# Performance work log

Measured on AMD Instinct MI355X. Metric: run time of the kernel, lower is better.

## Reference

```python
import jax, jax.numpy as jnp
import numpy as np
from jax import lax

B, S, D, E, K, MULT = 4, 2048, 1024, 1536, 4, 4
LN_EPS = 1e-5

def log_g(x):
    return jnp.where(x >= 0, jnp.log(jax.nn.relu(x) + 0.5), -jax.nn.softplus(-x))

def layer_norm(x, g, b):
    mu = jnp.mean(x, axis=-1, keepdims=True)
    var = jnp.mean((x - mu) ** 2, axis=-1, keepdims=True)
    return (x - mu) * lax.rsqrt(var + LN_EPS) * g + b

def setup_inputs() -> dict:
    key = jax.random.key(0)
    ks = jax.random.split(key, 16)
    s = lambda fan: 1.0 / np.sqrt(fan)
    inp = {
        'x': jax.random.normal(ks[0], (B, S, D), dtype=jnp.float32),
        'conv_dw_w': jax.random.uniform(ks[1], (D, 1, K), jnp.float32, -s(K), s(K)),
        'conv_dw_b': jax.random.uniform(ks[2], (D,), jnp.float32, -s(K), s(K)),
        'conv_pw_w': jax.random.uniform(ks[3], (D, D), jnp.float32, -s(D), s(D)),
        'conv_pw_b': jax.random.uniform(ks[4], (D,), jnp.float32, -s(D), s(D)),
        'ln1_g': jnp.ones((D,), jnp.float32),
        'ln1_b': jnp.zeros((D,), jnp.float32),
        'w_f': jax.random.uniform(ks[5], (E, D), jnp.float32, -s(D), s(D)),
        'w_i': jax.random.uniform(ks[6], (E, D), jnp.float32, -s(D), s(D)),
        'w_h': jax.random.uniform(ks[7], (E, D), jnp.float32, -s(D), s(D)),
        'w_down': jax.random.uniform(ks[8], (D, E), jnp.float32, -s(E), s(E)),
        'ln2_g': jnp.ones((D,), jnp.float32),
        'ln2_b': jnp.zeros((D,), jnp.float32),
        'mlp_w1': jax.random.uniform(ks[9], (MULT * D, D), jnp.float32, -s(D), s(D)),
        'mlp_b1': jax.random.uniform(ks[10], (MULT * D,), jnp.float32, -s(D), s(D)),
        'mlp_w2': jax.random.uniform(ks[11], (D, MULT * D), jnp.float32, -s(MULT * D), s(MULT * D)),
        'mlp_b2': jax.random.uniform(ks[12], (D,), jnp.float32, -s(MULT * D), s(MULT * D)),
    }
    return inp

def _forward(x, conv_dw_w, conv_dw_b, conv_pw_w, conv_pw_b, ln1_g, ln1_b,
             w_f, w_i, w_h, w_down, ln2_g, ln2_b, mlp_w1, mlp_b1, mlp_w2, mlp_b2):
    residual = x
    # causal depthwise conv + pointwise conv (channels-first over time)
    xc = jnp.transpose(x, (0, 2, 1))                       # (B, D, S)
    xc = jnp.pad(xc, ((0, 0), (0, 0), (K - 1, 0)))         # left causal pad
    dw = lax.conv_general_dilated(xc, conv_dw_w, (1,), 'VALID',
                                  feature_group_count=D,
                                  dimension_numbers=('NCH', 'OIH', 'NCH'))
    dw = dw + conv_dw_b[None, :, None]
    pw = jnp.einsum('bds,ed->bes', dw, conv_pw_w) + conv_pw_b[None, :, None]
    x = jnp.transpose(pw, (0, 2, 1)) + residual
    x = layer_norm(x, ln1_g, ln1_b)
    # minLSTM log-space parallel scan
    log_f = -jax.nn.softplus(-(x @ w_f.T))                 # (B, S, E)
    log_i = -jax.nn.softplus(-(x @ w_i.T))
    log_th = log_g(x @ w_h.T)
    log_h0 = jnp.full((B, 1, E), jnp.log(jnp.float32(0.5)), dtype=x.dtype)
    log_values = jnp.concatenate([log_h0, log_i + log_th], axis=1)   # (B, S+1, E)
    a_star = jnp.pad(jnp.cumsum(log_f, axis=1), ((0, 0), (1, 0), (0, 0)))
    log_h = a_star + lax.cumlogsumexp(log_values - a_star, axis=1)
    h = jnp.exp(log_h)[:, 1:]                              # (B, S, E)
    x = h @ w_down.T + residual
    x = layer_norm(x, ln2_g, ln2_b)
    # MLP (exact GELU like torch default); dropout with p=0 is identity
    hmid = jax.nn.gelu(x @ mlp_w1.T + mlp_b1, approximate=False)
    return hmid @ mlp_w2.T + mlp_b2

def reference(x, conv_dw_w, conv_dw_b, conv_pw_w, conv_pw_b, ln1_g, ln1_b,
              w_f, w_i, w_h, w_down, ln2_g, ln2_b, mlp_w1, mlp_b1, mlp_w2, mlp_b2):
    return _forward(x, conv_dw_w, conv_dw_b, conv_pw_w, conv_pw_b, ln1_g, ln1_b,
                    w_f, w_i, w_h, w_down, ln2_g, ln2_b, mlp_w1, mlp_b1, mlp_w2, mlp_b2)
```

## Files before the change

kernel.cpp:

```cpp
#include <hip/hip_runtime.h>
#include <hip/hip_bf16.h>
#include <math.h>

using bf16 = __hip_bfloat16;
typedef __attribute__((ext_vector_type(8))) short s8v;
typedef __attribute__((ext_vector_type(4))) float f32x4;

#define B_  4
#define S_  2048
#define D_  1024
#define E_  1536
#define M_  (B_*S_)
#define BE_ (B_*E_)
#define NCH 16
#define CHS (S_/NCH)

__device__ __forceinline__ float b2f(bf16 h) { return __bfloat162float(h); }
__device__ __forceinline__ bf16  f2b(float f) { return __float2bfloat16(f); }

struct __align__(8)  bh4 { bf16 h[4]; };

__device__ __forceinline__ void gld16(const void* g, void* l) {
  __builtin_amdgcn_global_load_lds((const __attribute__((address_space(1))) void*)g,
                                   (__attribute__((address_space(3))) void*)l, 16, 0, 0);
}

__global__ __launch_bounds__(256) void cvt_k(const float* __restrict__ s,
                                             bf16* __restrict__ d, int n)
{
  int i = (blockIdx.x * 256 + threadIdx.x) * 4;
  if (i < n) {
    float4 v = *(const float4*)(s + i);
    bh4 o;
    o.h[0] = f2b(v.x); o.h[1] = f2b(v.y); o.h[2] = f2b(v.z); o.h[3] = f2b(v.w);
    *(bh4*)(d + i) = o;
  }
}

__global__ __launch_bounds__(256) void dwconv_k(const float* __restrict__ x,
                                                const float* __restrict__ w,
                                                const float* __restrict__ bias,
                                                bf16* __restrict__ out)
{
  int m = blockIdx.x;
  int s = m & (S_ - 1);
  int d = threadIdx.x * 4;
  float wf[4][4];
#pragma unroll
  for (int i = 0; i < 4; ++i) {
    float4 wr = *(const float4*)(w + (d + i) * 4);
    wf[i][0] = wr.x; wf[i][1] = wr.y; wf[i][2] = wr.z; wf[i][3] = wr.w;
  }
  float4 bb = *(const float4*)(bias + d);
  float acc[4] = {bb.x, bb.y, bb.z, bb.w};
#pragma unroll
  for (int k = 0; k < 4; ++k) {
    if (s - 3 + k >= 0) {
      float4 xv = *(const float4*)(x + (size_t)(m - 3 + k) * D_ + d);
      acc[0] += xv.x * wf[0][k];
      acc[1] += xv.y * wf[1][k];
      acc[2] += xv.z * wf[2][k];
      acc[3] += xv.w * wf[3][k];
    }
  }
  bh4 ov;
#pragma unroll
  for (int i = 0; i < 4; ++i) ov.h[i] = f2b(acc[i]);
  *(bh4*)(out + (size_t)m * D_ + d) = ov;
}

template<int EPI>
__global__ __launch_bounds__(256) void gemm_ab(const bf16* __restrict__ A, int lda,
                                               const bf16* __restrict__ Bb, int ldb,
                                               const float* __restrict__ bias,
                                               const float* __restrict__ resid,
                                               bf16* outH, bf16* outH2, float* outF,
                                               int M, int N, int K)
{
  __shared__ __align__(16) bf16 lsA[128 * 64];
  __shared__ __align__(16) bf16 lsB[128 * 64];
  const int tid  = threadIdx.x;
  const int lane = tid & 63;
  const int wave = tid >> 6;
  const int m0 = blockIdx.y * 128, n0 = blockIdx.x * 128;
  const int wm = (wave >> 1) * 64, wn = (wave & 1) * 64;
  const int r = lane & 15, q = lane >> 4;
  const int sw = r & 7;
  f32x4 acc[4][4] = {};

  for (int k0 = 0; k0 < K; k0 += 64) {
#pragma unroll
    for (int i = 0; i < 4; ++i) {
      int c = i * 256 + tid;
      int row = c >> 3, cc = (c & 7) ^ (row & 7);
      gld16(A  + (size_t)(m0 + row) * lda + k0 + cc * 8, (char*)lsA + c * 16);
      gld16(Bb + (size_t)(n0 + row) * ldb + k0 + cc * 8, (char*)lsB + c * 16);
    }
    __syncthreads();
#pragma unroll
    for (int kk = 0; kk < 64; kk += 32) {
      const int j = (kk >> 3) + q;
      s8v af[4], bfr[4];
#pragma unroll
      for (int t = 0; t < 4; ++t) {
        af[t]  = *(const s8v*)((char*)lsA + (((wm + t * 16 + r) << 3) + (j ^ sw)) * 16);
        bfr[t] = *(const s8v*)((char*)lsB + (((wn + t * 16 + r) << 3) + (j ^ sw)) * 16);
      }
#pragma unroll
      for (int mi = 0; mi < 4; ++mi)
#pragma unroll
        for (int ni = 0; ni < 4; ++ni)
          acc[mi][ni] = __builtin_amdgcn_mfma_f32_16x16x32_bf16(af[mi], bfr[ni], acc[mi][ni], 0, 0, 0);
    }
    __syncthreads();
  }

#pragma unroll
  for (int mi = 0; mi < 4; ++mi) {
#pragma unroll
    for (int j = 0; j < 4; ++j) {
      int row = m0 + wm + mi * 16 + q * 4 + j;
#pragma unroll
      for (int ni = 0; ni < 4; ++ni) {
        int col = n0 + wn + ni * 16 + r;
        size_t idx = (size_t)row * N + col;
        float v = acc[mi][ni][j];
        if constexpr (EPI == 0) {
          outH[idx] = f2b(v + bias[col] + resid[idx]);
        } else if constexpr (EPI == 1) {
          if (col < 1536) outH [(size_t)row * 1536 + col]        = f2b(v);
          else            outH2[(size_t)row * 1536 + col - 1536] = f2b(v);
        } else if constexpr (EPI == 2) {
          float gh = (v >= 0.f) ? (v + 0.5f) : (1.f / (1.f + expf(-v)));
          float iv = 1.f / (1.f + expf(-b2f(outH[idx])));
          outH[idx] = f2b(gh * iv);
        } else if constexpr (EPI == 3) {
          outH[idx] = f2b(v + resid[idx]);
        } else if constexpr (EPI == 4) {
          float u = v + bias[col];
          outH[idx] = f2b(0.5f * u * (1.f + erff(u * 0.70710678118f)));
        } else {
          outF[idx] = v + bias[col];
        }
      }
    }
  }
}

__global__ __launch_bounds__(256) void ln_k(const bf16* __restrict__ y,
                                            const float* __restrict__ g,
                                            const float* __restrict__ b,
                                            bf16* __restrict__ out)
{
  __shared__ float sm[8];
  int row = blockIdx.x;
  bh4 v4 = ((const bh4*)(y + (size_t)row * D_))[threadIdx.x];
  float v0 = b2f(v4.h[0]), v1 = b2f(v4.h[1]), v2 = b2f(v4.h[2]), v3 = b2f(v4.h[3]);
  float s = v0 + v1 + v2 + v3;
#pragma unroll
  for (int o = 32; o; o >>= 1) s += __shfl_down(s, o);
  int lane = threadIdx.x & 63, w = threadIdx.x >> 6;
  if (lane == 0) sm[w] = s;
  __syncthreads();
  float mu = (sm[0] + sm[1] + sm[2] + sm[3]) * (1.f / D_);
  float d0 = v0 - mu, d1 = v1 - mu, d2 = v2 - mu, d3 = v3 - mu;
  float qq = d0 * d0 + d1 * d1 + d2 * d2 + d3 * d3;
#pragma unroll
  for (int o = 32; o; o >>= 1) qq += __shfl_down(qq, o);
  if (lane == 0) sm[4 + w] = qq;
  __syncthreads();
  float var = (sm[4] + sm[5] + sm[6] + sm[7]) * (1.f / D_);
  float inv = rsqrtf(var + 1e-5f);
  int c = threadIdx.x * 4;
  float4 gv = *(const float4*)(g + c);
  float4 bv = *(const float4*)(b + c);
  bh4 ov;
  ov.h[0] = f2b(d0 * inv * gv.x + bv.x);
  ov.h[1] = f2b(d1 * inv * gv.y + bv.y);
  ov.h[2] = f2b(d2 * inv * gv.z + bv.z);
  ov.h[3] = f2b(d3 * inv * gv.w + bv.w);
  *(bh4*)(out + (size_t)row * D_ + c) = ov;
}

__global__ __launch_bounds__(256) void scanA2_k(const bf16* __restrict__ fpre,
                                                const bf16* __restrict__ g,
                                                float* __restrict__ Fc, float* __restrict__ Gc)
{
  int gth = blockIdx.x * 256 + threadIdx.x;
  int c = gth / BE_, be = gth % BE_;
  int b = be / E_,  e = be % E_;
  size_t idx = (size_t)b * S_ * E_ + (size_t)c * CHS * E_ + e;
  float F = 1.f, G = 0.f;
  for (int sl = 0; sl < CHS; ++sl, idx += E_) {
    float fv = 1.f / (1.f + expf(-b2f(fpre[idx])));
    F *= fv;
    G = fv * G + b2f(g[idx]);
  }
  Fc[gth] = F; Gc[gth] = G;
}

__global__ __launch_bounds__(256) void scanB_k(const float* __restrict__ Fc,
                                               const float* __restrict__ Gc,
                                               float* __restrict__ hst)
{
  int be = blockIdx.x * 256 + threadIdx.x;
  float h = 0.5f;
#pragma unroll
  for (int c = 0; c < NCH; ++c) {
    hst[c * BE_ + be] = h;
    h = Fc[c * BE_ + be] * h + Gc[c * BE_ + be];
  }
}

__global__ __launch_bounds__(256) void scanC2_k(const bf16* __restrict__ fpre,
                                                bf16* g,
                                                const float* __restrict__ hst)
{
  int gth = blockIdx.x * 256 + threadIdx.x;
  int c = gth / BE_, be = gth % BE_;
  int b = be / E_,  e = be % E_;
  size_t idx = (size_t)b * S_ * E_ + (size_t)c * CHS * E_ + e;
  float h = hst[gth];
  for (int sl = 0; sl < CHS; ++sl, idx += E_) {
    float fv = 1.f / (1.f + expf(-b2f(fpre[idx])));
    h = fv * h + b2f(g[idx]);
    g[idx] = f2b(h);
  }
}

extern "C" void kernel_launch(void* const* d_in, const int* in_sizes, int n_in,
                              void* d_out, int out_size, void* d_ws, size_t ws_size,
                              hipStream_t stream)
{
  (void)in_sizes; (void)n_in; (void)out_size; (void)ws_size;
  const float* x      = (const float*)d_in[0];
  const float* cdw_w  = (const float*)d_in[1];
  const float* cdw_b  = (const float*)d_in[2];
  const float* cpw_w  = (const float*)d_in[3];
  const float* cpw_b  = (const float*)d_in[4];
  const float* ln1_g  = (const float*)d_in[5];
  const float* ln1_b  = (const float*)d_in[6];
  const float* w_f    = (const float*)d_in[7];
  const float* w_i    = (const float*)d_in[8];
  const float* w_h    = (const float*)d_in[9];
  const float* w_down = (const float*)d_in[10];
  const float* ln2_g  = (const float*)d_in[11];
  const float* ln2_b  = (const float*)d_in[12];
  const float* mlp_w1 = (const float*)d_in[13];
  const float* mlp_b1 = (const float*)d_in[14];
  const float* mlp_w2 = (const float*)d_in[15];
  const float* mlp_b2 = (const float*)d_in[16];
  char* ws = (char*)d_ws;
  float* outF = (float*)d_out;

  bf16* dw_buf = (bf16*)(ws + 0);
  bf16* xln    = (bf16*)(ws + 0);
  float* Fc    = (float*)(ws + 0);
  float* Gc    = (float*)(ws + 393216);
  float* hst   = (float*)(ws + 786432);
  bf16* yb     = (bf16*)(ws + 16777216);
  bf16* hmid   = (bf16*)(ws + 16777216);
  bf16* fpre   = (bf16*)(ws + 33554432);
  bf16* gvals  = (bf16*)(ws + 58720256);
  bf16* pwb    = (bf16*)(ws + 83886080);
  bf16* wfib   = (bf16*)(ws + 85983232);
  bf16* whb    = (bf16*)(ws + 92274688);
  bf16* wdb    = (bf16*)(ws + 95420416);
  bf16* w1b    = (bf16*)(ws + 98566144);
  bf16* w2b    = (bf16*)(ws + 106954752);

  cvt_k<<<(D_*D_)/1024,   256, 0, stream>>>(cpw_w,  pwb, D_*D_);
  cvt_k<<<(E_*D_)/1024,   256, 0, stream>>>(w_f,    wfib, E_*D_);
  cvt_k<<<(E_*D_)/1024,   256, 0, stream>>>(w_i,    wfib + E_*D_, E_*D_);
  cvt_k<<<(E_*D_)/1024,   256, 0, stream>>>(w_h,    whb, E_*D_);
  cvt_k<<<(D_*E_)/1024,   256, 0, stream>>>(w_down, wdb, D_*E_);
  cvt_k<<<(4*D_*D_)/1024, 256, 0, stream>>>(mlp_w1, w1b, 4*D_*D_);
  cvt_k<<<(4*D_*D_)/1024, 256, 0, stream>>>(mlp_w2, w2b, 4*D_*D_);

  dwconv_k<<<M_, 256, 0, stream>>>(x, cdw_w, cdw_b, dw_buf);
  gemm_ab<0><<<dim3(8, 64), 256, 0, stream>>>(dw_buf, D_, pwb, D_, cpw_b, x, yb, nullptr, nullptr, M_, D_, D_);
  ln_k<<<M_, 256, 0, stream>>>(yb, ln1_g, ln1_b, xln);
  gemm_ab<1><<<dim3(24, 64), 256, 0, stream>>>(xln, D_, wfib, D_, nullptr, nullptr, fpre, gvals, nullptr, M_, 3072, D_);
  gemm_ab<2><<<dim3(12, 64), 256, 0, stream>>>(xln, D_, whb, D_, nullptr, nullptr, gvals, nullptr, nullptr, M_, E_, D_);
  scanA2_k<<<(BE_*NCH)/256, 256, 0, stream>>>(fpre, gvals, Fc, Gc);
  scanB_k<<<BE_/256, 256, 0, stream>>>(Fc, Gc, hst);
  scanC2_k<<<(BE_*NCH)/256, 256, 0, stream>>>(fpre, gvals, hst);
  gemm_ab<3><<<dim3(8, 64), 256, 0, stream>>>(gvals, E_, wdb, E_, nullptr, x, yb, nullptr, nullptr, M_, D_, E_);
  ln_k<<<M_, 256, 0, stream>>>(yb, ln2_g, ln2_b, xln);
  gemm_ab<4><<<dim3(32, 64), 256, 0, stream>>>(xln, D_, w1b, D_, mlp_b1, nullptr, hmid, nullptr, nullptr, M_, 4*D_, D_);
  gemm_ab<5><<<dim3(8, 64), 256, 0, stream>>>(hmid, 4*D_, w2b, 4*D_, mlp_b2, nullptr, nullptr, nullptr, outF, M_, D_, 4*D_);
}
```

Before: 658.1 us.

## Add 256x256-tile 8-wave phased GEMM for gate and MLP-up projections

Introduces a new bf16 MFMA GEMM kernel with 256x256 block tiles, 512 threads, double-buffered LDS via direct global-to-LDS loads, and a four-phase inner loop. That loop interleaves the next tile's loads with MFMA work under raised wave priority. It replaces the earlier GEMM for the f/i, h and MLP-up projections to raise arithmetic intensity and overlap memory with compute. The cost is 128KB of LDS per block, limiting occupancy to one block per CU. Grid sizes of 384 and 192 blocks may also leave CUs idle or create tail waves.

```diff
diff --git a/kernel.cpp b/kernel.cpp
--- a/kernel.cpp
+++ b/kernel.cpp
@@ -147,6 +147,169 @@
   }
 }
 
+__device__ __forceinline__ void mfma_ph(f32x4 (*ac)[4], const s8v af[2][2], const s8v bf[4][2]) {
+  __builtin_amdgcn_s_setprio(1);
+#pragma unroll
+  for (int kc = 0; kc < 2; ++kc)
+#pragma unroll
+    for (int mm = 0; mm < 2; ++mm)
+#pragma unroll
+      for (int n = 0; n < 4; ++n)
+        ac[mm][n] = __builtin_amdgcn_mfma_f32_16x16x32_bf16(af[mm][kc], bf[n][kc], ac[mm][n], 0, 0, 0);
+  __builtin_amdgcn_s_setprio(0);
+}
+
+template<int EPI>
+__global__ __launch_bounds__(512, 2) void gemm8p(const bf16* __restrict__ A, int lda,
+                                                 const bf16* __restrict__ Bb, int ldb,
+                                                 const float* __restrict__ bias,
+                                                 const float* __restrict__ resid,
+                                                 bf16* outH, bf16* outH2, float* outF,
+                                                 int M, int N, int K)
+{
+  __shared__ __align__(16) bf16 lsA[2][256 * 64];
+  __shared__ __align__(16) bf16 lsB[2][256 * 64];
+  const int tid  = threadIdx.x;
+  const int lane = tid & 63;
+  const int wave = tid >> 6;
+  const int q = lane >> 4, r = lane & 15;
+  const int wm = (wave >> 2) * 128;
+  const int wn = (wave & 3) * 64;
+  const int s0 = q ^ (r & 7);
+  const int s0b  = s0 << 4;
+  const int s0b4 = (s0 ^ 4) << 4;
+  const int m0 = blockIdx.y * 256, n0 = blockIdx.x * 256;
+  const int NT = K >> 6;
+
+  f32x4 acc[8][4] = {};
+  s8v af[2][2], bf4[4][2];
+
+  auto stB = [&](int h, int tn, int nb) {
+#pragma unroll
+    for (int i = 0; i < 2; ++i) {
+      int c  = (i << 9) + tid;
+      int rw = (h << 7) + (c >> 3);
+      int cc = (c & 7) ^ ((c >> 3) & 7);
+      gld16(Bb + (unsigned)((n0 + rw) * ldb + (tn << 6) + (cc << 3)),
+            (char*)lsB[nb] + (((h << 10) + c) << 4));
+    }
+  };
+  auto stA = [&](int h, int tn, int nb) {
+#pragma unroll
+    for (int i = 0; i < 2; ++i) {
+      int c   = (i << 9) + tid;
+      int sub = c >> 3;
+      int rw  = (sub & 63) + ((sub >> 6) << 7) + (h << 6);
+      int cc  = (c & 7) ^ (sub & 7);
+      gld16(A + (unsigned)((m0 + rw) * lda + (tn << 6) + (cc << 3)),
+            (char*)lsA[nb] + (((rw << 3) + (c & 7)) << 4));
+    }
+  };
+
+  stB(0, 0, 0); stB(1, 0, 0); stA(0, 0, 0); stA(1, 0, 0);
+
+  for (int t = 0; t < NT; ++t) {
+    const int cb = t & 1, nb = cb ^ 1;
+    const int tn = (t + 1 < NT) ? t + 1 : t;
+    const char* lsAc = (const char*)lsA[cb];
+    const char* lsBc = (const char*)lsB[cb];
+
+    asm volatile("s_waitcnt vmcnt(2)" ::: "memory");
+    __builtin_amdgcn_s_barrier();
+
+    {
+      const char* bb_ = lsBc + ((wn + r) << 7);
+#pragma unroll
+      for (int n = 0; n < 4; ++n) {
+        bf4[n][0] = *(const s8v*)(bb_ + n * 2048 + s0b);
+        bf4[n][1] = *(const s8v*)(bb_ + n * 2048 + s0b4);
+      }
+      const char* ab_ = lsAc + ((wm + r) << 7);
+      af[0][0] = *(const s8v*)(ab_ + s0b);
+      af[0][1] = *(const s8v*)(ab_ + s0b4);
+      af[1][0] = *(const s8v*)(ab_ + 2048 + s0b);
+      af[1][1] = *(const s8v*)(ab_ + 2048 + s0b4);
+    }
+    stB(0, tn, nb);
+    __builtin_amdgcn_s_barrier();
+    asm volatile("s_waitcnt lgkmcnt(0)" ::: "memory");
+    mfma_ph(&acc[0], af, bf4);
+    __builtin_amdgcn_s_barrier();
+
+    {
+      const char* ab_ = lsAc + ((wm + 32 + r) << 7);
+      af[0][0] = *(const s8v*)(ab_ + s0b);
+      af[0][1] = *(const s8v*)(ab_ + s0b4);
+      af[1][0] = *(const s8v*)(ab_ + 2048 + s0b);
+      af[1][1] = *(const s8v*)(ab_ + 2048 + s0b4);
+    }
+    stB(1, tn, nb);
+    __builtin_amdgcn_s_barrier();
+    asm volatile("s_waitcnt lgkmcnt(0)" ::: "memory");
+    mfma_ph(&acc[2], af, bf4);
+    asm volatile("s_waitcnt vmcnt(4)" ::: "memory");
+    __builtin_amdgcn_s_barrier();
+
+    {
+      const char* ab_ = lsAc + ((wm + 64 + r) << 7);
+      af[0][0] = *(const s8v*)(ab_ + s0b);
+      af[0][1] = *(const s8v*)(ab_ + s0b4);
+      af[1][0] = *(const s8v*)(ab_ + 2048 + s0b);
+      af[1][1] = *(const s8v*)(ab_ + 2048 + s0b4);
+    }
+    stA(0, tn, nb);
+    __builtin_amdgcn_s_barrier();
+    asm volatile("s_waitcnt lgkmcnt(0)" ::: "memory");
+    mfma_ph(&acc[4], af, bf4);
+    __builtin_amdgcn_s_barrier();
+
+    {
+      const char* ab_ = lsAc + ((wm + 96 + r) << 7);
+      af[0][0] = *(const s8v*)(ab_ + s0b);
+      af[0][1] = *(const s8v*)(ab_ + s0b4);
+      af[1][0] = *(const s8v*)(ab_ + 2048 + s0b);
+      af[1][1] = *(const s8v*)(ab_ + 2048 + s0b4);
+    }
+    stA(1, tn, nb);
+    __builtin_amdgcn_s_barrier();
+    asm volatile("s_waitcnt lgkmcnt(0)" ::: "memory");
+    mfma_ph(&acc[6], af, bf4);
+    __builtin_amdgcn_s_barrier();
+  }
+  asm volatile("s_waitcnt vmcnt(0)" ::: "memory");
+
+#pragma unroll
+  for (int mi = 0; mi < 8; ++mi) {
+#pragma unroll
+    for (int j = 0; j < 4; ++j) {
+      int row = m0 + wm + mi * 16 + q * 4 + j;
+#pragma unroll
+      for (int ni = 0; ni < 4; ++ni) {
+        int col = n0 + wn + ni * 16 + r;
+        size_t idx = (size_t)row * N + col;
+        float v = acc[mi][ni][j];
+        if constexpr (EPI == 0) {
+          outH[idx] = f2b(v + bias[col] + resid[idx]);
+        } else if constexpr (EPI == 1) {
+          if (col < 1536) outH [(size_t)row * 1536 + col]        = f2b(v);
+          else            outH2[(size_t)row * 1536 + col - 1536] = f2b(v);
+        } else if constexpr (EPI == 2) {
+          float gh = (v >= 0.f) ? (v + 0.5f) : (1.f / (1.f + expf(-v)));
+          float iv = 1.f / (1.f + expf(-b2f(outH[idx])));
+          outH[idx] = f2b(gh * iv);
+        } else if constexpr (EPI == 3) {
+          outH[idx] = f2b(v + resid[idx]);
+        } else if constexpr (EPI == 4) {
+          float u = v + bias[col];
+          outH[idx] = f2b(0.5f * u * (1.f + erff(u * 0.70710678118f)));
+        } else {
+          outF[idx] = v + bias[col];
+        }
+      }
+    }
+  }
+}
+
 __global__ __launch_bounds__(256) void ln_k(const bf16* __restrict__ y,
                                             const float* __restrict__ g,
                                             const float* __restrict__ b,
@@ -280,13 +443,13 @@
   dwconv_k<<<M_, 256, 0, stream>>>(x, cdw_w, cdw_b, dw_buf);
   gemm_ab<0><<<dim3(8, 64), 256, 0, stream>>>(dw_buf, D_, pwb, D_, cpw_b, x, yb, nullptr, nullptr, M_, D_, D_);
   ln_k<<<M_, 256, 0, stream>>>(yb, ln1_g, ln1_b, xln);
-  gemm_ab<1><<<dim3(24, 64), 256, 0, stream>>>(xln, D_, wfib, D_, nullptr, nullptr, fpre, gvals, nullptr, M_, 3072, D_);
-  gemm_ab<2><<<dim3(12, 64), 256, 0, stream>>>(xln, D_, whb, D_, nullptr, nullptr, gvals, nullptr, nullptr, M_, E_, D_);
+  gemm8p<1><<<dim3(12, 32), 512, 0, stream>>>(xln, D_, wfib, D_, nullptr, nullptr, fpre, gvals, nullptr, M_, 3072, D_);
+  gemm8p<2><<<dim3(6, 32),  512, 0, stream>>>(xln, D_, whb, D_, nullptr, nullptr, gvals, nullptr, nullptr, M_, E_, D_);
   scanA2_k<<<(BE_*NCH)/256, 256, 0, stream>>>(fpre, gvals, Fc, Gc);
   scanB_k<<<BE_/256, 256, 0, stream>>>(Fc, Gc, hst);
   scanC2_k<<<(BE_*NCH)/256, 256, 0, stream>>>(fpre, gvals, hst);
   gemm_ab<3><<<dim3(8, 64), 256, 0, stream>>>(gvals, E_, wdb, E_, nullptr, x, yb, nullptr, nullptr, M_, D_, E_);
   ln_k<<<M_, 256, 0, stream>>>(yb, ln2_g, ln2_b, xln);
-  gemm_ab<4><<<dim3(32, 64), 256, 0, stream>>>(xln, D_, w1b, D_, mlp_b1, nullptr, hmid, nullptr, nullptr, M_, 4*D_, D_);
+  gemm8p<4><<<dim3(16, 32), 512, 0, stream>>>(xln, D_, w1b, D_, mlp_b1, nullptr, hmid, nullptr, nullptr, M_, 4*D_, D_);
   gemm_ab<5><<<dim3(8, 64), 256, 0, stream>>>(hmid, 4*D_, w2b, 4*D_, mlp_b2, nullptr, nullptr, nullptr, outF, M_, D_, 4*D_);
 }
```

New measurement: 865.1 us. 1.31x slower.

## Double-buffer GEMM LDS loads with split A halves and merge weight converts

Applied to the files above, without the earlier changes.

The GEMM now double-buffers its LDS tiles. The next k-tile's B and A halves are issued through global_load_lds while MFMAs run on the current tile, and explicit vmcnt waits and barriers replace the two __syncthreads per iteration. The A tile load is split into two halves, interleaved with two MFMA phases under raised wave priority. The seven weight-conversion launches are merged into one kernel that dispatches on the flat index, which relies on the weight buffers being laid out contiguously in the workspace. Doubling LDS to 64KB per block and asking for 2 blocks per SM via launch bounds puts pressure on occupancy and registers.

```diff
diff --git a/kernel.cpp b/kernel.cpp
--- a/kernel.cpp
+++ b/kernel.cpp
@@ -25,16 +25,32 @@
                                    (__attribute__((address_space(3))) void*)l, 16, 0, 0);
 }
 
-__global__ __launch_bounds__(256) void cvt_k(const float* __restrict__ s,
-                                             bf16* __restrict__ d, int n)
-{
-  int i = (blockIdx.x * 256 + threadIdx.x) * 4;
-  if (i < n) {
-    float4 v = *(const float4*)(s + i);
-    bh4 o;
-    o.h[0] = f2b(v.x); o.h[1] = f2b(v.y); o.h[2] = f2b(v.z); o.h[3] = f2b(v.w);
-    *(bh4*)(d + i) = o;
-  }
+__global__ __launch_bounds__(256) void cvt7_k(const float* __restrict__ s0,
+                                              const float* __restrict__ s1,
+                                              const float* __restrict__ s2,
+                                              const float* __restrict__ s3,
+                                              const float* __restrict__ s4,
+                                              const float* __restrict__ s5,
+                                              const float* __restrict__ s6,
+                                              bf16* __restrict__ d)
+{
+  size_t i = ((size_t)blockIdx.x * 256 + threadIdx.x) * 4;
+  const float* s; size_t off;
+  if (i < 4194304) {
+    if (i < 1048576)      { s = s0; off = 0; }
+    else if (i < 2621440) { s = s1; off = 1048576; }
+    else                  { s = s2; off = 2621440; }
+  } else if (i < 7340032) {
+    if (i < 5767168)      { s = s3; off = 4194304; }
+    else                  { s = s4; off = 5767168; }
+  } else {
+    if (i < 11534336)     { s = s5; off = 7340032; }
+    else                  { s = s6; off = 11534336; }
+  }
+  float4 v = *(const float4*)(s + (i - off));
+  bh4 o;
+  o.h[0] = f2b(v.x); o.h[1] = f2b(v.y); o.h[2] = f2b(v.z); o.h[3] = f2b(v.w);
+  *(bh4*)(d + i) = o;
 }
 
 __global__ __launch_bounds__(256) void dwconv_k(const float* __restrict__ x,
@@ -70,15 +86,15 @@
 }
 
 template<int EPI>
-__global__ __launch_bounds__(256) void gemm_ab(const bf16* __restrict__ A, int lda,
-                                               const bf16* __restrict__ Bb, int ldb,
-                                               const float* __restrict__ bias,
-                                               const float* __restrict__ resid,
-                                               bf16* outH, bf16* outH2, float* outF,
-                                               int M, int N, int K)
-{
-  __shared__ __align__(16) bf16 lsA[128 * 64];
-  __shared__ __align__(16) bf16 lsB[128 * 64];
+__global__ __launch_bounds__(256, 2) void gemm_ab(const bf16* __restrict__ A, int lda,
+                                                  const bf16* __restrict__ Bb, int ldb,
+                                                  const float* __restrict__ bias,
+                                                  const float* __restrict__ resid,
+                                                  bf16* outH, bf16* outH2, float* outF,
+                                                  int M, int N, int K)
+{
+  __shared__ __align__(16) bf16 lsA[2][128 * 64];
+  __shared__ __align__(16) bf16 lsB[2][128 * 64];
   const int tid  = threadIdx.x;
   const int lane = tid & 63;
   const int wave = tid >> 6;
@@ -88,32 +104,79 @@
   const int sw = r & 7;
   f32x4 acc[4][4] = {};
 
-  for (int k0 = 0; k0 < K; k0 += 64) {
+  auto stB = [&](int tn, int nb) {
 #pragma unroll
     for (int i = 0; i < 4; ++i) {
       int c = i * 256 + tid;
       int row = c >> 3, cc = (c & 7) ^ (row & 7);
-      gld16(A  + (size_t)(m0 + row) * lda + k0 + cc * 8, (char*)lsA + c * 16);
-      gld16(Bb + (size_t)(n0 + row) * ldb + k0 + cc * 8, (char*)lsB + c * 16);
+      gld16(Bb + (size_t)(n0 + row) * ldb + tn * 64 + cc * 8, (char*)lsB[nb] + c * 16);
     }
-    __syncthreads();
-#pragma unroll
-    for (int kk = 0; kk < 64; kk += 32) {
-      const int j = (kk >> 3) + q;
-      s8v af[4], bfr[4];
-#pragma unroll
-      for (int t = 0; t < 4; ++t) {
-        af[t]  = *(const s8v*)((char*)lsA + (((wm + t * 16 + r) << 3) + (j ^ sw)) * 16);
-        bfr[t] = *(const s8v*)((char*)lsB + (((wn + t * 16 + r) << 3) + (j ^ sw)) * 16);
-      }
-#pragma unroll
-      for (int mi = 0; mi < 4; ++mi)
+  };
+  auto stA = [&](int h, int tn, int nb) {
+#pragma unroll
+    for (int i = 0; i < 2; ++i) {
+      int c = i * 256 + tid;
+      int sub = c >> 3;
+      int rw = (sub & 31) + ((sub >> 5) << 6) + h * 32;
+      int cc = (c & 7) ^ (sub & 7);
+      gld16(A + (size_t)(m0 + rw) * lda + tn * 64 + cc * 8,
+            (char*)lsA[nb] + (((rw << 3) + (c & 7)) << 4));
+    }
+  };
+
+  const int NT = K >> 6;
+  stB(0, 0); stA(0, 0, 0); stA(1, 0, 0);
+
+  for (int t = 0; t < NT; ++t) {
+    const int cb = t & 1, nb = cb ^ 1;
+    const int tn = (t + 1 < NT) ? (t + 1) : t;
+    const char* la = (const char*)lsA[cb];
+    const char* lb = (const char*)lsB[cb];
+
+    asm volatile("s_waitcnt vmcnt(2)" ::: "memory");
+    __builtin_amdgcn_s_barrier();
+    stB(tn, nb); stA(0, tn, nb);
+
+    s8v bfr[4][2], af[2][2];
+#pragma unroll
+    for (int ni = 0; ni < 4; ++ni)
+#pragma unroll
+      for (int kc = 0; kc < 2; ++kc)
+        bfr[ni][kc] = *(const s8v*)(lb + ((((wn + ni * 16 + r) << 3) + ((q + kc * 4) ^ sw)) << 4));
+#pragma unroll
+    for (int mi = 0; mi < 2; ++mi)
+#pragma unroll
+      for (int kc = 0; kc < 2; ++kc)
+        af[mi][kc] = *(const s8v*)(la + ((((wm + mi * 16 + r) << 3) + ((q + kc * 4) ^ sw)) << 4));
+    __builtin_amdgcn_s_setprio(1);
+#pragma unroll
+    for (int kc = 0; kc < 2; ++kc)
+#pragma unroll
+      for (int mi = 0; mi < 2; ++mi)
 #pragma unroll
         for (int ni = 0; ni < 4; ++ni)
-          acc[mi][ni] = __builtin_amdgcn_mfma_f32_16x16x32_bf16(af[mi], bfr[ni], acc[mi][ni], 0, 0, 0);
-    }
-    __syncthreads();
-  }
+          acc[mi][ni] = __builtin_amdgcn_mfma_f32_16x16x32_bf16(af[mi][kc], bfr[ni][kc], acc[mi][ni], 0, 0, 0);
+    __builtin_amdgcn_s_setprio(0);
+
+    asm volatile("s_waitcnt vmcnt(6)" ::: "memory");
+    __builtin_amdgcn_s_barrier();
+    stA(1, tn, nb);
+#pragma unroll
+    for (int mi = 0; mi < 2; ++mi)
+#pragma unroll
+      for (int kc = 0; kc < 2; ++kc)
+        af[mi][kc] = *(const s8v*)(la + ((((wm + (mi + 2) * 16 + r) << 3) + ((q + kc * 4) ^ sw)) << 4));
+    __builtin_amdgcn_s_setprio(1);
+#pragma unroll
+    for (int kc = 0; kc < 2; ++kc)
+#pragma unroll
+      for (int mi = 0; mi < 2; ++mi)
+#pragma unroll
+        for (int ni = 0; ni < 4; ++ni)
+          acc[mi + 2][ni] = __builtin_amdgcn_mfma_f32_16x16x32_bf16(af[mi][kc], bfr[ni][kc], acc[mi + 2][ni], 0, 0, 0);
+    __builtin_amdgcn_s_setprio(0);
+  }
+  asm volatile("s_waitcnt vmcnt(0)" ::: "memory");
 
 #pragma unroll
   for (int mi = 0; mi < 4; ++mi) {
@@ -269,13 +332,7 @@
   bf16* w1b    = (bf16*)(ws + 98566144);
   bf16* w2b    = (bf16*)(ws + 106954752);
 
-  cvt_k<<<(D_*D_)/1024,   256, 0, stream>>>(cpw_w,  pwb, D_*D_);
-  cvt_k<<<(E_*D_)/1024,   256, 0, stream>>>(w_f,    wfib, E_*D_);
-  cvt_k<<<(E_*D_)/1024,   256, 0, stream>>>(w_i,    wfib + E_*D_, E_*D_);
-  cvt_k<<<(E_*D_)/1024,   256, 0, stream>>>(w_h,    whb, E_*D_);
-  cvt_k<<<(D_*E_)/1024,   256, 0, stream>>>(w_down, wdb, D_*E_);
-  cvt_k<<<(4*D_*D_)/1024, 256, 0, stream>>>(mlp_w1, w1b, 4*D_*D_);
-  cvt_k<<<(4*D_*D_)/1024, 256, 0, stream>>>(mlp_w2, w2b, 4*D_*D_);
+  cvt7_k<<<15360, 256, 0, stream>>>(cpw_w, w_f, w_i, w_h, w_down, mlp_w1, mlp_w2, pwb);
 
   dwconv_k<<<M_, 256, 0, stream>>>(x, cdw_w, cdw_b, dw_buf);
   gemm_ab<0><<<dim3(8, 64), 256, 0, stream>>>(dw_buf, D_, pwb, D_, cpw_b, x, yb, nullptr, nullptr, M_, D_, D_);
```

Result: slower. 723.5 us (+9.9%).

## Add 128x256 wide GEMM tile for large-N GEMMs and fuse weight conversions

Applied to the files above, without the earlier changes.

Adds a 512-thread GEMM kernel with a 128x256 output tile, where 8 waves share one A tile, and uses it for the fused f/i projection, the h projection and the first MLP GEMM. The wider tile is meant to cut redundant A-tile global loads and raise MFMA work per barrier. It also merges the seven weight fp32-to-bf16 conversion launches into one kernel with range-based source selection, reducing launch overhead. The larger LDS footprint (48KB) and fewer blocks may reduce occupancy or leave the grid unevenly spread across CUs.

```diff
diff --git a/kernel.cpp b/kernel.cpp
--- a/kernel.cpp
+++ b/kernel.cpp
@@ -25,16 +25,32 @@
                                    (__attribute__((address_space(3))) void*)l, 16, 0, 0);
 }
 
-__global__ __launch_bounds__(256) void cvt_k(const float* __restrict__ s,
-                                             bf16* __restrict__ d, int n)
-{
-  int i = (blockIdx.x * 256 + threadIdx.x) * 4;
-  if (i < n) {
-    float4 v = *(const float4*)(s + i);
-    bh4 o;
-    o.h[0] = f2b(v.x); o.h[1] = f2b(v.y); o.h[2] = f2b(v.z); o.h[3] = f2b(v.w);
-    *(bh4*)(d + i) = o;
-  }
+__global__ __launch_bounds__(256) void cvt7_k(const float* __restrict__ s0,
+                                              const float* __restrict__ s1,
+                                              const float* __restrict__ s2,
+                                              const float* __restrict__ s3,
+                                              const float* __restrict__ s4,
+                                              const float* __restrict__ s5,
+                                              const float* __restrict__ s6,
+                                              bf16* __restrict__ d)
+{
+  size_t i = ((size_t)blockIdx.x * 256 + threadIdx.x) * 4;
+  const float* s; size_t off;
+  if (i < 4194304) {
+    if (i < 1048576)      { s = s0; off = 0; }
+    else if (i < 2621440) { s = s1; off = 1048576; }
+    else                  { s = s2; off = 2621440; }
+  } else if (i < 7340032) {
+    if (i < 5767168)      { s = s3; off = 4194304; }
+    else                  { s = s4; off = 5767168; }
+  } else {
+    if (i < 11534336)     { s = s5; off = 7340032; }
+    else                  { s = s6; off = 11534336; }
+  }
+  float4 v = *(const float4*)(s + (i - off));
+  bh4 o;
+  o.h[0] = f2b(v.x); o.h[1] = f2b(v.y); o.h[2] = f2b(v.z); o.h[3] = f2b(v.w);
+  *(bh4*)(d + i) = o;
 }
 
 __global__ __launch_bounds__(256) void dwconv_k(const float* __restrict__ x,
@@ -67,6 +83,32 @@
 #pragma unroll
   for (int i = 0; i < 4; ++i) ov.h[i] = f2b(acc[i]);
   *(bh4*)(out + (size_t)m * D_ + d) = ov;
+}
+
+template<int EPI>
+__device__ __forceinline__ void epi_store(float v, int row, int col, int N,
+                                          const float* __restrict__ bias,
+                                          const float* __restrict__ resid,
+                                          bf16* outH, bf16* outH2, float* outF)
+{
+  size_t idx = (size_t)row * N + col;
+  if constexpr (EPI == 0) {
+    outH[idx] = f2b(v + bias[col] + resid[idx]);
+  } else if constexpr (EPI == 1) {
+    if (col < 1536) outH [(size_t)row * 1536 + col]        = f2b(v);
+    else            outH2[(size_t)row * 1536 + col - 1536] = f2b(v);
+  } else if constexpr (EPI == 2) {
+    float gh = (v >= 0.f) ? (v + 0.5f) : (1.f / (1.f + expf(-v)));
+    float iv = 1.f / (1.f + expf(-b2f(outH[idx])));
+    outH[idx] = f2b(gh * iv);
+  } else if constexpr (EPI == 3) {
+    outH[idx] = f2b(v + resid[idx]);
+  } else if constexpr (EPI == 4) {
+    float u = v + bias[col];
+    outH[idx] = f2b(0.5f * u * (1.f + erff(u * 0.70710678118f)));
+  } else {
+    outF[idx] = v + bias[col];
+  }
 }
 
 template<int EPI>
@@ -116,35 +158,77 @@
   }
 
 #pragma unroll
-  for (int mi = 0; mi < 4; ++mi) {
+  for (int mi = 0; mi < 4; ++mi)
 #pragma unroll
     for (int j = 0; j < 4; ++j) {
       int row = m0 + wm + mi * 16 + q * 4 + j;
 #pragma unroll
-      for (int ni = 0; ni < 4; ++ni) {
-        int col = n0 + wn + ni * 16 + r;
-        size_t idx = (size_t)row * N + col;
-        float v = acc[mi][ni][j];
-        if constexpr (EPI == 0) {
-          outH[idx] = f2b(v + bias[col] + resid[idx]);
-        } else if constexpr (EPI == 1) {
-          if (col < 1536) outH [(size_t)row * 1536 + col]        = f2b(v);
-          else            outH2[(size_t)row * 1536 + col - 1536] = f2b(v);
-        } else if constexpr (EPI == 2) {
-          float gh = (v >= 0.f) ? (v + 0.5f) : (1.f / (1.f + expf(-v)));
-          float iv = 1.f / (1.f + expf(-b2f(outH[idx])));
-          outH[idx] = f2b(gh * iv);
-        } else if constexpr (EPI == 3) {
-          outH[idx] = f2b(v + resid[idx]);
-        } else if constexpr (EPI == 4) {
-          float u = v + bias[col];
-          outH[idx] = f2b(0.5f * u * (1.f + erff(u * 0.70710678118f)));
-        } else {
-          outF[idx] = v + bias[col];
-        }
+      for (int ni = 0; ni < 4; ++ni)
+        epi_store<EPI>(acc[mi][ni][j], row, n0 + wn + ni * 16 + r, N, bias, resid, outH, outH2, outF);
+    }
+}
+
+template<int EPI>
+__global__ __launch_bounds__(512, 4) void gemm_wide(const bf16* __restrict__ A, int lda,
+                                                    const bf16* __restrict__ Bb, int ldb,
+                                                    const float* __restrict__ bias,
+                                                    const float* __restrict__ resid,
+                                                    bf16* outH, bf16* outH2, float* outF,
+                                                    int M, int N, int K)
+{
+  __shared__ __align__(16) bf16 lsA[128 * 64];
+  __shared__ __align__(16) bf16 lsB[256 * 64];
+  const int tid  = threadIdx.x;
+  const int lane = tid & 63;
+  const int wave = tid >> 6;
+  const int m0 = blockIdx.y * 128, n0 = blockIdx.x * 256;
+  const int wm = (wave >> 2) * 64;
+  const int wn = (wave & 3) * 64;
+  const int r = lane & 15, q = lane >> 4;
+  const int sw = r & 7;
+  f32x4 acc[4][4] = {};
+
+  for (int k0 = 0; k0 < K; k0 += 64) {
+#pragma unroll
+    for (int i = 0; i < 2; ++i) {
+      int c = i * 512 + tid;
+      int row = c >> 3, cc = (c & 7) ^ (row & 7);
+      gld16(A + (size_t)(m0 + row) * lda + k0 + cc * 8, (char*)lsA + c * 16);
+    }
+#pragma unroll
+    for (int i = 0; i < 4; ++i) {
+      int c = i * 512 + tid;
+      int row = c >> 3, cc = (c & 7) ^ (row & 7);
+      gld16(Bb + (size_t)(n0 + row) * ldb + k0 + cc * 8, (char*)lsB + c * 16);
+    }
+    __syncthreads();
+#pragma unroll
+    for (int kk = 0; kk < 64; kk += 32) {
+      const int j = (kk >> 3) + q;
+      s8v af[4], bfr[4];
+#pragma unroll
+      for (int t = 0; t < 4; ++t) {
+        af[t]  = *(const s8v*)((char*)lsA + (((wm + t * 16 + r) << 3) + (j ^ sw)) * 16);
+        bfr[t] = *(const s8v*)((char*)lsB + (((wn + t * 16 + r) << 3) + (j ^ sw)) * 16);
       }
-    }
-  }
+#pragma unroll
+      for (int mi = 0; mi < 4; ++mi)
+#pragma unroll
+        for (int ni = 0; ni < 4; ++ni)
+          acc[mi][ni] = __builtin_amdgcn_mfma_f32_16x16x32_bf16(af[mi], bfr[ni], acc[mi][ni], 0, 0, 0);
+    }
+    __syncthreads();
+  }
+
+#pragma unroll
+  for (int mi = 0; mi < 4; ++mi)
+#pragma unroll
+    for (int j = 0; j < 4; ++j) {
+      int row = m0 + wm + mi * 16 + q * 4 + j;
+#pragma unroll
+      for (int ni = 0; ni < 4; ++ni)
+        epi_store<EPI>(acc[mi][ni][j], row, n0 + wn + ni * 16 + r, N, bias, resid, outH, outH2, outF);
+    }
 }
 
 __global__ __launch_bounds__(256) void ln_k(const bf16* __restrict__ y,
@@ -269,24 +353,18 @@
   bf16* w1b    = (bf16*)(ws + 98566144);
   bf16* w2b    = (bf16*)(ws + 106954752);
 
-  cvt_k<<<(D_*D_)/1024,   256, 0, stream>>>(cpw_w,  pwb, D_*D_);
-  cvt_k<<<(E_*D_)/1024,   256, 0, stream>>>(w_f,    wfib, E_*D_);
-  cvt_k<<<(E_*D_)/1024,   256, 0, stream>>>(w_i,    wfib + E_*D_, E_*D_);
-  cvt_k<<<(E_*D_)/1024,   256, 0, stream>>>(w_h,    whb, E_*D_);
-  cvt_k<<<(D_*E_)/1024,   256, 0, stream>>>(w_down, wdb, D_*E_);
-  cvt_k<<<(4*D_*D_)/1024, 256, 0, stream>>>(mlp_w1, w1b, 4*D_*D_);
-  cvt_k<<<(4*D_*D_)/1024, 256, 0, stream>>>(mlp_w2, w2b, 4*D_*D_);
+  cvt7_k<<<15360, 256, 0, stream>>>(cpw_w, w_f, w_i, w_h, w_down, mlp_w1, mlp_w2, pwb);
 
   dwconv_k<<<M_, 256, 0, stream>>>(x, cdw_w, cdw_b, dw_buf);
   gemm_ab<0><<<dim3(8, 64), 256, 0, stream>>>(dw_buf, D_, pwb, D_, cpw_b, x, yb, nullptr, nullptr, M_, D_, D_);
   ln_k<<<M_, 256, 0, stream>>>(yb, ln1_g, ln1_b, xln);
-  gemm_ab<1><<<dim3(24, 64), 256, 0, stream>>>(xln, D_, wfib, D_, nullptr, nullptr, fpre, gvals, nullptr, M_, 3072, D_);
-  gemm_ab<2><<<dim3(12, 64), 256, 0, stream>>>(xln, D_, whb, D_, nullptr, nullptr, gvals, nullptr, nullptr, M_, E_, D_);
+  gemm_wide<1><<<dim3(12, 64), 512, 0, stream>>>(xln, D_, wfib, D_, nullptr, nullptr, fpre, gvals, nullptr, M_, 3072, D_);
+  gemm_wide<2><<<dim3(6, 64),  512, 0, stream>>>(xln, D_, whb, D_, nullptr, nullptr, gvals, nullptr, nullptr, M_, E_, D_);
   scanA2_k<<<(BE_*NCH)/256, 256, 0, stream>>>(fpre, gvals, Fc, Gc);
   scanB_k<<<BE_/256, 256, 0, stream>>>(Fc, Gc, hst);
   scanC2_k<<<(BE_*NCH)/256, 256, 0, stream>>>(fpre, gvals, hst);
   gemm_ab<3><<<dim3(8, 64), 256, 0, stream>>>(gvals, E_, wdb, E_, nullptr, x, yb, nullptr, nullptr, M_, D_, E_);
   ln_k<<<M_, 256, 0, stream>>>(yb, ln2_g, ln2_b, xln);
-  gemm_ab<4><<<dim3(32, 64), 256, 0, stream>>>(xln, D_, w1b, D_, mlp_b1, nullptr, hmid, nullptr, nullptr, M_, 4*D_, D_);
+  gemm_wide<4><<<dim3(16, 64), 512, 0, stream>>>(xln, D_, w1b, D_, mlp_b1, nullptr, hmid, nullptr, nullptr, M_, 4*D_, D_);
   gemm_ab<5><<<dim3(8, 64), 256, 0, stream>>>(hmid, 4*D_, w2b, 4*D_, mlp_b2, nullptr, nullptr, nullptr, outF, M_, D_, 4*D_);
 }
```

Measured after the change: 668.9 us. About the same (+1.6%).
